# Kernel optimization log

Hardware: AMD Instinct MI355X
Metric: run time of the kernel (lower is better)

## Reference

```python
import jax, jax.numpy as jnp
from jax import lax
import numpy as np

EPS = 1e-5

def _quant(w):
    # BitNet-style binarization: sign(w) scaled by mean(|w|), with STE (identity grad)
    alpha = jnp.mean(jnp.abs(w))
    wq = jnp.sign(w) * alpha
    return w + lax.stop_gradient(wq - w)

def _bn(x, gamma, beta, axes):
    mean = jnp.mean(x, axis=axes, keepdims=True)
    var = jnp.var(x, axis=axes, keepdims=True)
    shape = [1] * x.ndim
    shape[1] = x.shape[1]
    return (x - mean) * lax.rsqrt(var + EPS) * gamma.reshape(shape) + beta.reshape(shape)

def _conv(x, w):
    return lax.conv_general_dilated(x, w, window_strides=(1, 1), padding=((1, 1), (1, 1)),
                                    dimension_numbers=('NCHW', 'OIHW', 'NCHW'))

def _maxpool2(x):
    return lax.reduce_window(x, -jnp.inf, lax.max, (1, 1, 2, 2), (1, 1, 2, 2), 'VALID')

def setup_inputs() -> dict:
    key = jax.random.key(0)
    ks = jax.random.split(key, 5)
    return {
        'x': jax.random.normal(ks[0], (1024, 3, 32, 32), jnp.float32),
        'w1': jax.random.normal(ks[1], (64, 3, 3, 3), jnp.float32) * 0.1,
        'g1': jnp.ones((64,), jnp.float32), 'b1': jnp.zeros((64,), jnp.float32),
        'w2': jax.random.normal(ks[2], (128, 64, 3, 3), jnp.float32) * 0.05,
        'g2': jnp.ones((128,), jnp.float32), 'b2': jnp.zeros((128,), jnp.float32),
        'wfc1': jax.random.normal(ks[3], (256, 8192), jnp.float32) * 0.02,
        'g3': jnp.ones((256,), jnp.float32), 'b3': jnp.zeros((256,), jnp.float32),
        'wfc2': jax.random.normal(ks[4], (10, 256), jnp.float32) * 0.1,
    }

def reference(x, w1, g1, b1, w2, g2, b2, wfc1, g3, b3, wfc2):
    h = _conv(x, _quant(w1))                 # [B,64,32,32]
    h = _maxpool2(jax.nn.relu(_bn(h, g1, b1, (0, 2, 3))))  # [B,64,16,16]
    h = _conv(h, _quant(w2))                 # [B,128,16,16]
    h = _maxpool2(jax.nn.relu(_bn(h, g2, b2, (0, 2, 3))))  # [B,128,8,8]
    h = h.reshape(h.shape[0], -1)            # [B,8192]
    h = h @ _quant(wfc1).T                   # [B,256]
    h = jax.nn.relu(_bn(h, g3, b3, (0,)))
    return h @ _quant(wfc2).T                # [B,10]
```

## Files before the change

kernel.cpp:

```cpp
#include <hip/hip_runtime.h>
#include <stdint.h>

typedef unsigned short u16;
typedef unsigned int u32;
typedef __attribute__((ext_vector_type(8))) short s8v;
typedef __attribute__((ext_vector_type(4))) float f4v;
typedef __attribute__((ext_vector_type(8))) u16 u16x8;
typedef __attribute__((ext_vector_type(4))) u16 u16x4;

__device__ __forceinline__ float bf2f(u16 u){
  union { u32 i; float f; } v; v.i = ((u32)u) << 16; return v.f;
}
__device__ __forceinline__ u16 f2bf(float f){
  union { float f; u32 i; } v; v.f = f;
  u32 i = v.i;
  return (u16)((i + 0x7fffu + ((i >> 16) & 1u)) >> 16);
}
__device__ __forceinline__ float sgnf(float w){
  return (w > 0.f) ? 1.f : ((w < 0.f) ? -1.f : 0.f);
}
__device__ __forceinline__ u16 sgn_bf(float w){
  return (w > 0.f) ? (u16)0x3F80 : ((w < 0.f) ? (u16)0xBF80 : (u16)0);
}

#define GLL16(gaddr, laddr) __builtin_amdgcn_global_load_lds( \
    (const __attribute__((address_space(1))) void*)(gaddr),   \
    (__attribute__((address_space(3))) void*)(laddr), 16, 0, 0)

__global__ __launch_bounds__(256) void k_signgen_small(const float* __restrict__ w1, const float* __restrict__ w2,
                                                       const float* __restrict__ wfc2,
                                                       u16* __restrict__ qw1b, u16* __restrict__ qw2b,
                                                       float* __restrict__ qwfc2, float* __restrict__ partials){
  int i = blockIdx.x * 256 + threadIdx.x;
  float av = 0.f; int slot;
  if (i < 73728){
    int j = i & 7, lane = (i >> 3) & 63, fid = i >> 9;
    int s = fid >> 4, ks = (fid >> 3) & 1, nt = fid & 7;
    int co = (lane & 15)*8 + nt;
    int c = ks*32 + (lane >> 4)*8 + j;
    float wv = w2[((size_t)co*64 + c)*9 + s];
    qw2b[i] = sgn_bf(wv);
    av = fabsf(wv); slot = 1;
  } else if (i < 73728 + 2048){
    int i3 = i - 73728;
    int j = i3 & 7, lane = (i3 >> 3) & 63, nt = i3 >> 9;
    int co = nt*16 + (lane & 15);
    int k = (lane >> 4)*8 + j;
    if (k < 27){
      float wv = w1[co*27 + k];
      qw1b[i3] = sgn_bf(wv);
      av = fabsf(wv);
    } else qw1b[i3] = (u16)0;
    slot = 0;
  } else {
    int i4 = i - (73728 + 2048);
    float wv = wfc2[i4];
    qwfc2[i4] = sgnf(wv);
    av = fabsf(wv); slot = 3;
  }
  #pragma unroll
  for (int off = 32; off > 0; off >>= 1) av += __shfl_xor(av, off);
  if ((threadIdx.x & 63) == 0) atomicAdd(partials + slot*256 + (blockIdx.x & 255), av);
}

__global__ __launch_bounds__(256) void k_fc1gen(const float* __restrict__ wfc1, u16* __restrict__ qfc1b,
                                                float* __restrict__ partials){
  __shared__ u16 tile[128*72];
  int co = blockIdx.x, t = threadIdx.x;
  const float4* src = (const float4*)(wfc1 + (size_t)co*8192);
  float av = 0.f;
  #pragma unroll
  for (int p = 0; p < 8; ++p){
    int k4 = t + p*256;
    float4 v = src[k4];
    int c = k4 >> 4, px = (k4 & 15)*4;
    u16* d = tile + c*72 + px;
    d[0] = sgn_bf(v.x); d[1] = sgn_bf(v.y); d[2] = sgn_bf(v.z); d[3] = sgn_bf(v.w);
    av += fabsf(v.x) + fabsf(v.y) + fabsf(v.z) + fabsf(v.w);
  }
  #pragma unroll
  for (int off = 32; off > 0; off >>= 1) av += __shfl_xor(av, off);
  if ((t & 63) == 0) atomicAdd(partials + 2*256 + (co & 255), av);
  __syncthreads();
  int co4 = co >> 4, co15 = co & 15;
  #pragma unroll
  for (int p = 0; p < 4; ++p){
    int m = t + p*256;
    int px = m >> 4, jj = m & 15;
    int kstep = px*4 + (jj >> 2), l16 = jj & 3;
    u16x8 o;
    #pragma unroll
    for (int u = 0; u < 8; ++u) o[u] = tile[(jj*8 + u)*72 + px];
    *(u16x8*)(qfc1b + ((size_t)(kstep*16 + co4)*512 + (l16*16 + co15)*8)) = o;
  }
}

__global__ void k_red4(const float* __restrict__ partials, float* __restrict__ absum){
  int t = threadIdx.x, w = t >> 6, lane = t & 63;
  const float* p = partials + w*256;
  float s = p[lane] + p[lane + 64] + p[lane + 128] + p[lane + 192];
  #pragma unroll
  for (int off = 32; off > 0; off >>= 1) s += __shfl_xor(s, off);
  if (lane == 0) absum[w] = s;
}

__global__ __launch_bounds__(256) void k_conv1m(const float* __restrict__ x, const u16* __restrict__ qw1b,
                                                const float* __restrict__ absum, u16* __restrict__ p1raw,
                                                float* __restrict__ gs, float* __restrict__ gq){
  __shared__ float xs[3*34*36];
  __shared__ __align__(16) u16 acol[256*40];
  __shared__ float ls1[64], ls2[64];
  int n = blockIdx.x, t = threadIdx.x;
  if (t < 64){ ls1[t] = 0.f; ls2[t] = 0.f; }
  for (int i = t; i < 3672; i += 256) xs[i] = 0.f;
  __syncthreads();
  const float4* xg = (const float4*)(x + (size_t)n * 3072);
  for (int i = t; i < 768; i += 256){
    float4 v = xg[i];
    int ci = i >> 8, rem = i & 255, y = rem >> 3, xq = (rem & 7) * 4;
    int base = ci*1224 + (y+1)*36 + 2 + xq;
    xs[base+0] = v.x; xs[base+1] = v.y; xs[base+2] = v.z; xs[base+3] = v.w;
  }
  int w = t >> 6, lane = t & 63, l15 = lane & 15, q = lane >> 4;
  const s8v* bp = (const s8v*)qw1b;
  s8v bf[4];
  #pragma unroll
  for (int nt = 0; nt < 4; ++nt) bf[nt] = bp[nt*64 + lane];
  float alpha = absum[0] * (1.f/1728.f);
  u16* p1img = p1raw + (size_t)n * 16384;
  float s1v[4], s2v[4];
  #pragma unroll
  for (int nt = 0; nt < 4; ++nt){ s1v[nt] = 0.f; s2v[nt] = 0.f; }
  for (int chunk = 0; chunk < 4; ++chunk){
    __syncthreads();
    {
      int mg = chunk*256 + t;
      int g = mg >> 2, s = mg & 3;
      int iy = 2*(g >> 4) + (s >> 1), ix = 2*(g & 15) + (s & 1);
      const float* xb = xs + iy*36 + ix + 1;
      u32 pk2[16];
      #pragma unroll
      for (int kk = 0; kk < 16; ++kk){
        int k0 = 2*kk, k1 = 2*kk + 1;
        u32 lo = (k0 < 27) ? (u32)f2bf(xb[(k0/9)*1224 + ((k0%9)/3)*36 + (k0%3)]) : 0u;
        u32 hi = (k1 < 27) ? (u32)f2bf(xb[(k1/9)*1224 + ((k1%9)/3)*36 + (k1%3)]) : 0u;
        pk2[kk] = lo | (hi << 16);
      }
      u32* ar = (u32*)(acol + t*40);
      #pragma unroll
      for (int v = 0; v < 4; ++v)
        *(uint4*)(ar + v*4) = make_uint4(pk2[v*4], pk2[v*4+1], pk2[v*4+2], pk2[v*4+3]);
    }
    __syncthreads();
    #pragma unroll
    for (int i = 0; i < 4; ++i){
      int tl = w*4 + i;
      s8v av = *(const s8v*)(acol + (tl*16 + l15)*40 + q*8);
      int g = chunk*64 + tl*4 + q;
      u16* drow = p1img + g*64 + l15;
      #pragma unroll
      for (int nt = 0; nt < 4; ++nt){
        f4v c = (f4v)(0.0f);
        c = __builtin_amdgcn_mfma_f32_16x16x32_bf16(av, bf[nt], c, 0, 0, 0);
        s1v[nt] += c[0] + c[1] + c[2] + c[3];
        s2v[nt] += c[0]*c[0] + c[1]*c[1] + c[2]*c[2] + c[3]*c[3];
        float pm = fmaxf(fmaxf(c[0], c[1]), fmaxf(c[2], c[3]));
        drow[nt*16] = f2bf(pm * alpha);
      }
    }
  }
  #pragma unroll
  for (int nt = 0; nt < 4; ++nt){
    s1v[nt] += __shfl_xor(s1v[nt], 16); s1v[nt] += __shfl_xor(s1v[nt], 32);
    s2v[nt] += __shfl_xor(s2v[nt], 16); s2v[nt] += __shfl_xor(s2v[nt], 32);
  }
  if (q == 0){
    #pragma unroll
    for (int nt = 0; nt < 4; ++nt){
      atomicAdd(&ls1[nt*16 + l15], s1v[nt]);
      atomicAdd(&ls2[nt*16 + l15], s2v[nt]);
    }
  }
  __syncthreads();
  if (t < 64){
    atomicAdd(gs + t, ls1[t] * alpha);
    atomicAdd(gq + t, ls2[t] * alpha * alpha);
  }
}

__global__ __launch_bounds__(512, 4) void k_conv2m(const u16* __restrict__ p1raw, const u16* __restrict__ qw2b,
                                                   const float* __restrict__ absum,
                                                   const float* __restrict__ s1, const float* __restrict__ q1,
                                                   const float* __restrict__ g1, const float* __restrict__ b1,
                                                   u16* __restrict__ p2raw,
                                                   float* __restrict__ gs, float* __restrict__ gq){
  __shared__ __align__(16) u16 img[16384];
  __shared__ __align__(16) u16 bstage[3][4096];
  int n = blockIdx.x, t = threadIdx.x;
  int c0 = (t & 7) * 8;
  float scv[8], biv[8];
  #pragma unroll
  for (int j = 0; j < 8; ++j){
    float m = s1[c0+j] * (1.f/1048576.f);
    float var = q1[c0+j] * (1.f/1048576.f) - m*m;
    float sc = g1[c0+j] * rsqrtf(var + 1e-5f);
    scv[j] = sc; biv[j] = b1[c0+j] - m*sc;
  }
  const u16* src = p1raw + (size_t)n * 16384;
  #pragma unroll
  for (int i = 0; i < 4; ++i){
    int id = i*512 + t;
    int px = id >> 3, unit = id & 7;
    int su = unit ^ (px & 7);
    u16x8 v = *(const u16x8*)(src + id*8);
    u16x8 o;
    #pragma unroll
    for (int j = 0; j < 8; ++j)
      o[j] = f2bf(fmaxf(bf2f(v[j]) * scv[j] + biv[j], 0.f));
    *(u16x8*)(img + px*64 + su*8) = o;
  }
  int w = t >> 6, lane = t & 63, l15 = lane & 15, q = lane >> 4;
  int wr = w >> 1, wc = w & 1;
  const char* bsrc = (const char*)qw2b;
  {
    const char* g = bsrc + w*1024 + lane*16;
    char* l = ((char*)bstage[0]) + w*1024;
    GLL16(g, l);
  }
  __syncthreads();
  f4v acc[4][4];
  #pragma unroll
  for (int a = 0; a < 4; ++a)
    #pragma unroll
    for (int b = 0; b < 4; ++b) acc[a][b] = (f4v)(0.0f);
  for (int p = 0; p < 18; ++p){
    int s = p >> 1, ks = p & 1;
    int dy = s / 3, dx = s - dy*3;
    int xv = l15 + dx - 1;
    bool vx = (xv >= 0) && (xv < 16);
    int xc = min(max(xv, 0), 15);
    if (p < 17){
      const char* g = bsrc + (size_t)(p + 1)*8192 + w*1024 + lane*16;
      char* l = ((char*)bstage[(p + 1) % 3]) + w*1024;
      GLL16(g, l);
      asm volatile("s_waitcnt vmcnt(1)" ::: "memory");
    } else {
      asm volatile("s_waitcnt vmcnt(0)" ::: "memory");
    }
    __builtin_amdgcn_s_barrier();
    asm volatile("" ::: "memory");
    const u16* bb = bstage[p % 3];
    s8v bf[4];
    #pragma unroll
    for (int nt = 0; nt < 4; ++nt) bf[nt] = *(const s8v*)(bb + ((wc*4 + nt)*64 + lane)*8);
    __builtin_amdgcn_s_setprio(1);
    #pragma unroll
    for (int mt = 0; mt < 4; ++mt){
      int yv = wr*4 + mt + dy - 1;
      if (yv >= 0 && yv <= 15){
        int px = yv*16 + xc;
        int su = (ks*4 + q) ^ (px & 7);
        s8v av = *(const s8v*)(img + px*64 + su*8);
        if (!vx) av = (s8v)(short)0;
        #pragma unroll
        for (int nt = 0; nt < 4; ++nt)
          acc[mt][nt] = __builtin_amdgcn_mfma_f32_16x16x32_bf16(av, bf[nt], acc[mt][nt], 0, 0, 0);
      }
    }
    __builtin_amdgcn_s_setprio(0);
  }
  float alpha = absum[1] * (1.f/73728.f);
  float s1v[4], s2v[4];
  #pragma unroll
  for (int nt = 0; nt < 4; ++nt){ s1v[nt] = 0.f; s2v[nt] = 0.f; }
  #pragma unroll
  for (int mp = 0; mp < 2; ++mp){
    #pragma unroll
    for (int rp = 0; rp < 2; ++rp){
      u16x4 pk;
      #pragma unroll
      for (int nt = 0; nt < 4; ++nt){
        float v0 = acc[2*mp][nt][2*rp]     * alpha;
        float v1 = acc[2*mp][nt][2*rp+1]   * alpha;
        float v2 = acc[2*mp+1][nt][2*rp]   * alpha;
        float v3 = acc[2*mp+1][nt][2*rp+1] * alpha;
        s1v[nt] += v0 + v1 + v2 + v3;
        s2v[nt] += v0*v0 + v1*v1 + v2*v2 + v3*v3;
        pk[nt] = f2bf(fmaxf(fmaxf(v0, v1), fmaxf(v2, v3)));
      }
      int opx = (wr*2 + mp)*8 + (q*2 + rp);
      *(u16x4*)(p2raw + ((size_t)n*64 + opx)*128 + l15*8 + wc*4) = pk;
    }
  }
  #pragma unroll
  for (int nt = 0; nt < 4; ++nt){
    s1v[nt] += __shfl_xor(s1v[nt], 16); s1v[nt] += __shfl_xor(s1v[nt], 32);
    s2v[nt] += __shfl_xor(s2v[nt], 16); s2v[nt] += __shfl_xor(s2v[nt], 32);
  }
  __syncthreads();
  float* ls = (float*)img;
  if (t < 256) ls[t] = 0.f;
  __syncthreads();
  if (q == 0){
    #pragma unroll
    for (int nt = 0; nt < 4; ++nt){
      atomicAdd(&ls[l15*8 + wc*4 + nt], s1v[nt]);
      atomicAdd(&ls[128 + l15*8 + wc*4 + nt], s2v[nt]);
    }
  }
  __syncthreads();
  if (t < 128){ atomicAdd(gs + t, ls[t]); atomicAdd(gq + t, ls[128 + t]); }
}

__global__ __launch_bounds__(256) void k_bn2(u16* __restrict__ p2,
                                             const float* __restrict__ s2, const float* __restrict__ q2,
                                             const float* __restrict__ g2, const float* __restrict__ b2){
  size_t i = (size_t)blockIdx.x * 256 + threadIdx.x;
  int c0 = ((int)(i & 15)) * 8;
  float scv[8], biv[8];
  #pragma unroll
  for (int j = 0; j < 8; ++j){
    float m = s2[c0+j] * (1.f/262144.f);
    float var = q2[c0+j] * (1.f/262144.f) - m*m;
    float sc = g2[c0+j] * rsqrtf(var + 1e-5f);
    scv[j] = sc; biv[j] = b2[c0+j] - m*sc;
  }
  u16x8 v = *(u16x8*)(p2 + i*8);
  u16x8 o;
  #pragma unroll
  for (int j = 0; j < 8; ++j)
    o[j] = f2bf(fmaxf(bf2f(v[j]) * scv[j] + biv[j], 0.f));
  *(u16x8*)(p2 + i*8) = o;
}

__global__ __launch_bounds__(256) void k_fc1m(const u16* __restrict__ p2, const u16* __restrict__ qfc1b,
                                              const float* __restrict__ absum, float* __restrict__ h3p){
  int t = threadIdx.x;
  int bm = blockIdx.x, bn = blockIdx.y, kb = blockIdx.z;
  int w = t >> 6, lane = t & 63, l15 = lane & 15, q = lane >> 4;
  int rowbase = bm*128 + (w >> 1)*64;
  int ntb = bn*8 + (w & 1)*4;
  const s8v* bp = (const s8v*)qfc1b;
  f4v acc[4][4];
  #pragma unroll
  for (int a = 0; a < 4; ++a)
    #pragma unroll
    for (int b = 0; b < 4; ++b) acc[a][b] = (f4v)(0.0f);
  #pragma unroll 2
  for (int ks = 0; ks < 16; ++ks){
    int kst = kb*16 + ks;
    s8v bf[4], af[4];
    #pragma unroll
    for (int nt = 0; nt < 4; ++nt) bf[nt] = bp[(kst*16 + ntb + nt)*64 + lane];
    #pragma unroll
    for (int mt = 0; mt < 4; ++mt)
      af[mt] = *(const s8v*)(p2 + (size_t)(rowbase + mt*16 + l15)*8192 + kst*32 + q*8);
    #pragma unroll
    for (int mt = 0; mt < 4; ++mt)
      #pragma unroll
      for (int nt = 0; nt < 4; ++nt)
        acc[mt][nt] = __builtin_amdgcn_mfma_f32_16x16x32_bf16(af[mt], bf[nt], acc[mt][nt], 0, 0, 0);
  }
  float alpha = absum[2] * (1.f/2097152.f);
  float* dst = h3p + (size_t)kb * 262144;
  #pragma unroll
  for (int mt = 0; mt < 4; ++mt)
    #pragma unroll
    for (int nt = 0; nt < 4; ++nt){
      int col = (ntb + nt)*16 + l15;
      #pragma unroll
      for (int r = 0; r < 4; ++r)
        dst[(size_t)(rowbase + mt*16 + q*4 + r)*256 + col] = acc[mt][nt][r] * alpha;
    }
}

__global__ __launch_bounds__(256) void k_fin3f(const float* __restrict__ h3p, float* __restrict__ h3,
                                               float* __restrict__ s3, float* __restrict__ q3){
  int jb = blockIdx.x, ns = blockIdx.y, t = threadIdx.x;
  int jj = t & 31, nn = t >> 5;
  int j = jb*32 + jj;
  float s1 = 0.f, s2 = 0.f;
  for (int i = nn; i < 128; i += 8){
    int n = i*8 + ns;
    float v = 0.f;
    #pragma unroll 8
    for (int kb = 0; kb < 16; ++kb) v += h3p[(size_t)kb*262144 + n*256 + j];
    h3[n*256 + j] = v;
    s1 += v; s2 += v*v;
  }
  __shared__ float l1[256], l2[256];
  l1[t] = s1; l2[t] = s2;
  __syncthreads();
  if (t < 32){
    float a = 0.f, b = 0.f;
    #pragma unroll
    for (int k = 0; k < 8; ++k){ a += l1[t+32*k]; b += l2[t+32*k]; }
    atomicAdd(s3 + jb*32 + t, a); atomicAdd(q3 + jb*32 + t, b);
  }
}

__global__ __launch_bounds__(64) void k_fc2(const float* __restrict__ h3, const float* __restrict__ qwfc2,
                                            const float* __restrict__ absum,
                                            const float* __restrict__ s3, const float* __restrict__ q3,
                                            const float* __restrict__ g3, const float* __restrict__ b3,
                                            float* __restrict__ out){
  int n = blockIdx.x, lane = threadIdx.x;
  float a[4];
  #pragma unroll
  for (int i = 0; i < 4; ++i){
    int j = lane + 64*i;
    float m = s3[j] * (1.f/1024.f);
    float var = q3[j] * (1.f/1024.f) - m*m;
    float sc = g3[j] * rsqrtf(var + 1e-5f);
    float v = h3[(size_t)n*256 + j] * sc + (b3[j] - m*sc);
    a[i] = fmaxf(v, 0.f);
  }
  float alpha = absum[3] * (1.f/2560.f);
  #pragma unroll
  for (int k = 0; k < 10; ++k){
    float p = 0.f;
    #pragma unroll
    for (int i = 0; i < 4; ++i) p += a[i] * qwfc2[k*256 + lane + 64*i];
    #pragma unroll
    for (int off = 32; off > 0; off >>= 1) p += __shfl_down(p, off);
    if (lane == 0) out[n*10 + k] = p * alpha;
  }
}

extern "C" void kernel_launch(void* const* d_in, const int* in_sizes, int n_in,
                              void* d_out, int out_size, void* d_ws, size_t ws_size,
                              hipStream_t stream){
  (void)in_sizes; (void)n_in; (void)out_size; (void)ws_size;
  const float* x    = (const float*)d_in[0];
  const float* w1   = (const float*)d_in[1];
  const float* g1   = (const float*)d_in[2];
  const float* b1   = (const float*)d_in[3];
  const float* w2   = (const float*)d_in[4];
  const float* g2   = (const float*)d_in[5];
  const float* b2   = (const float*)d_in[6];
  const float* wfc1 = (const float*)d_in[7];
  const float* g3   = (const float*)d_in[8];
  const float* b3   = (const float*)d_in[9];
  const float* wfc2 = (const float*)d_in[10];
  float* out = (float*)d_out;

  float* wsf = (float*)d_ws;
  char*  wsb = (char*)d_ws;
  float* absum = wsf;
  float* s1 = wsf + 16;   float* q1 = wsf + 80;
  float* s2 = wsf + 144;  float* q2 = wsf + 272;
  float* s3 = wsf + 1024; float* q3 = wsf + 1280;
  float* partials = wsf + 2048;
  u16*   qw1b  = (u16*)(wsf + 4096);
  u16*   qw2b  = (u16*)(wsb + (64u << 10));
  float* qwfc2 = (float*)(wsb + (256u << 10));
  float* h3    = (float*)(wsb + (1ull << 20));
  u16*   qfc1b = (u16*)(wsb + (2ull << 20));
  u16*   p1t   = (u16*)(wsb + (8ull << 20) + 4096);
  u16*   p2    = (u16*)(wsb + (112ull << 20));
  float* h3p   = (float*)(wsb + (128ull << 20));

  hipMemsetAsync(wsf, 0, 3072 * sizeof(float), stream);
  k_signgen_small<<<306, 256, 0, stream>>>(w1, w2, wfc2, qw1b, qw2b, qwfc2, partials);
  k_fc1gen<<<256, 256, 0, stream>>>(wfc1, qfc1b, partials);
  k_red4<<<1, 256, 0, stream>>>(partials, absum);
  k_conv1m<<<1024, 256, 0, stream>>>(x, qw1b, absum, p1t, s1, q1);
  k_conv2m<<<1024, 512, 0, stream>>>(p1t, qw2b, absum, s1, q1, g1, b1, p2, s2, q2);
  k_bn2<<<4096, 256, 0, stream>>>(p2, s2, q2, g2, b2);
  k_fc1m<<<dim3(8, 2, 16), 256, 0, stream>>>(p2, qfc1b, absum, h3p);
  k_fin3f<<<dim3(8, 8), 256, 0, stream>>>(h3p, h3, s3, q3);
  k_fc2<<<1024, 64, 0, stream>>>(h3, qwfc2, absum, s3, q3, g3, b3, out);
}
```

Measured before the change: 235.5 us.

## Pad conv2 image in LDS and load weights directly to registers

The conv2 kernel now stores the activation image in LDS with zeroed left/right padding columns (18-wide rows), so the per-lane x-boundary clamp and masking disappear. The triple-buffered LDS staging of weight fragments through global_load_lds with per-step barriers is dropped. Weights are instead double-buffered in registers straight from global memory, and the 18-step loop is fully unrolled. This removes 18 block barriers and the LDS round trip for weights, at the cost of more VGPRs and redundant global/L2 weight reads per wave.

```diff
diff --git a/kernel.cpp b/kernel.cpp
--- a/kernel.cpp
+++ b/kernel.cpp
@@ -22,10 +22,6 @@
 __device__ __forceinline__ u16 sgn_bf(float w){
   return (w > 0.f) ? (u16)0x3F80 : ((w < 0.f) ? (u16)0xBF80 : (u16)0);
 }
-
-#define GLL16(gaddr, laddr) __builtin_amdgcn_global_load_lds( \
-    (const __attribute__((address_space(1))) void*)(gaddr),   \
-    (__attribute__((address_space(3))) void*)(laddr), 16, 0, 0)
 
 __global__ __launch_bounds__(256) void k_signgen_small(const float* __restrict__ w1, const float* __restrict__ w2,
                                                        const float* __restrict__ wfc2,
@@ -194,8 +190,7 @@
                                                    const float* __restrict__ g1, const float* __restrict__ b1,
                                                    u16* __restrict__ p2raw,
                                                    float* __restrict__ gs, float* __restrict__ gq){
-  __shared__ __align__(16) u16 img[16384];
-  __shared__ __align__(16) u16 bstage[3][4096];
+  __shared__ __align__(16) u16 img[288*64];
   int n = blockIdx.x, t = threadIdx.x;
   int c0 = (t & 7) * 8;
   float scv[8], biv[8];
@@ -206,11 +201,19 @@
     float sc = g1[c0+j] * rsqrtf(var + 1e-5f);
     scv[j] = sc; biv[j] = b1[c0+j] - m*sc;
   }
+  if (t < 256){
+    int cl = t >> 7, y = (t >> 3) & 15, unit = t & 7;
+    int px = y*18 + cl*17;
+    int su = unit ^ (px & 7);
+    *(u16x8*)(img + px*64 + su*8) = (u16x8)(u16)0;
+  }
   const u16* src = p1raw + (size_t)n * 16384;
   #pragma unroll
   for (int i = 0; i < 4; ++i){
     int id = i*512 + t;
-    int px = id >> 3, unit = id & 7;
+    int p0 = id >> 3, unit = id & 7;
+    int y = p0 >> 4, x = p0 & 15;
+    int px = y*18 + x + 1;
     int su = unit ^ (px & 7);
     u16x8 v = *(const u16x8*)(src + id*8);
     u16x8 o;
@@ -219,52 +222,38 @@
       o[j] = f2bf(fmaxf(bf2f(v[j]) * scv[j] + biv[j], 0.f));
     *(u16x8*)(img + px*64 + su*8) = o;
   }
+  __syncthreads();
   int w = t >> 6, lane = t & 63, l15 = lane & 15, q = lane >> 4;
   int wr = w >> 1, wc = w & 1;
-  const char* bsrc = (const char*)qw2b;
-  {
-    const char* g = bsrc + w*1024 + lane*16;
-    char* l = ((char*)bstage[0]) + w*1024;
-    GLL16(g, l);
-  }
-  __syncthreads();
+  const s8v* bp = (const s8v*)qw2b;
   f4v acc[4][4];
   #pragma unroll
   for (int a = 0; a < 4; ++a)
     #pragma unroll
     for (int b = 0; b < 4; ++b) acc[a][b] = (f4v)(0.0f);
+  s8v bf[2][4];
+  #pragma unroll
+  for (int nt = 0; nt < 4; ++nt) bf[0][nt] = bp[(wc*4 + nt)*64 + lane];
+  #pragma unroll
   for (int p = 0; p < 18; ++p){
-    int s = p >> 1, ks = p & 1;
-    int dy = s / 3, dx = s - dy*3;
-    int xv = l15 + dx - 1;
-    bool vx = (xv >= 0) && (xv < 16);
-    int xc = min(max(xv, 0), 15);
+    const int s = p >> 1, ks = p & 1;
+    const int dy = s / 3, dx = s % 3;
     if (p < 17){
-      const char* g = bsrc + (size_t)(p + 1)*8192 + w*1024 + lane*16;
-      char* l = ((char*)bstage[(p + 1) % 3]) + w*1024;
-      GLL16(g, l);
-      asm volatile("s_waitcnt vmcnt(1)" ::: "memory");
-    } else {
-      asm volatile("s_waitcnt vmcnt(0)" ::: "memory");
-    }
-    __builtin_amdgcn_s_barrier();
-    asm volatile("" ::: "memory");
-    const u16* bb = bstage[p % 3];
-    s8v bf[4];
-    #pragma unroll
-    for (int nt = 0; nt < 4; ++nt) bf[nt] = *(const s8v*)(bb + ((wc*4 + nt)*64 + lane)*8);
+      #pragma unroll
+      for (int nt = 0; nt < 4; ++nt)
+        bf[(p + 1) & 1][nt] = bp[((p + 1)*8 + wc*4 + nt)*64 + lane];
+    }
     __builtin_amdgcn_s_setprio(1);
     #pragma unroll
     for (int mt = 0; mt < 4; ++mt){
       int yv = wr*4 + mt + dy - 1;
       if (yv >= 0 && yv <= 15){
-        int px = yv*16 + xc;
+        int px = yv*18 + l15 + dx;
         int su = (ks*4 + q) ^ (px & 7);
         s8v av = *(const s8v*)(img + px*64 + su*8);
-        if (!vx) av = (s8v)(short)0;
         #pragma unroll
         for (int nt = 0; nt < 4; ++nt)
-          acc[mt][nt] = __builtin_amdgcn_mfma_f32_16x16x32_bf16(av, bf[nt], acc[mt][nt], 0, 0, 0);
+          acc[mt][nt] = __builtin_amdgcn_mfma_f32_16x16x32_bf16(av, bf[p & 1][nt], acc[mt][nt], 0, 0, 0);
       }
     }
     __builtin_amdgcn_s_setprio(0);
```

Result: slower. 243.5 us (+3.4%).
